# Kernel optimization log

Hardware: AMD Instinct MI355X
Metric: run time of the kernel (lower is better)

Reference implementation:

```python
import jax, jax.numpy as jnp
import numpy as np

BATCH, NEURONS, N_FEAT, IN_DIM, OUT_DIM = 256, 1024, 1024, 256, 128


def setup_inputs() -> dict:
    key = jax.random.key(0)
    kx, kg, kv, kw = jax.random.split(key, 4)
    x = jax.random.normal(kx, (BATCH, N_FEAT, IN_DIM), dtype=jnp.float32)
    G = jax.random.normal(kg, (NEURONS, N_FEAT), dtype=jnp.float32)
    # Original initializes v, w to zeros; use randn so outputs/grads are non-trivial.
    v = jax.random.normal(kv, (NEURONS, IN_DIM, OUT_DIM), dtype=jnp.float32)
    w = jax.random.normal(kw, (NEURONS, IN_DIM, OUT_DIM), dtype=jnp.float32)
    return {"x": x, "G": G, "v": v, "w": w}


def reference(x, G, v, w):
    # Original math: out[i,m] = sum_{j,k,l} G[j,k] * x[i,k,l] * (v - w)[j,l,m]
    # Reordered contraction: first G @ x (sum over feature axis k),
    # avoiding the quadratic (batch, neurons, n, in_dim) intermediate.
    Gx = jnp.einsum('jk,ikl->ijl', G, x)          # (batch, neurons, in_dim)
    return jnp.einsum('ijl,jlm->im', Gx, v - w)    # (batch, out_dim)
```

## Files before the change

### kernel.cpp

```cpp
#include <hip/hip_runtime.h>
#include <hip/hip_bf16.h>


typedef __attribute__((ext_vector_type(8))) short bf16x8;
typedef __attribute__((ext_vector_type(4))) float f32x4;

#define AS1C(p) ((const __attribute__((address_space(1))) void*)(p))
#define AS3(p)  ((__attribute__((address_space(3))) void*)(p))
#define FENCE() asm volatile("" ::: "memory")

__device__ __forceinline__ unsigned short f2bf(float f) {
    unsigned u = __float_as_uint(f);
    unsigned r = u + 0x7fffu + ((u >> 16) & 1u);
    return (unsigned short)(r >> 16);
}

__global__ void prep_G(const float* __restrict__ G, unsigned short* __restrict__ Gt) {
    __shared__ float tile[32][33];
    int k0 = blockIdx.x * 32, j0 = blockIdx.y * 32;
    int tx = threadIdx.x, ty = threadIdx.y;
    #pragma unroll
    for (int r = 0; r < 32; r += 8)
        tile[ty + r][tx] = G[(size_t)(j0 + ty + r) * 1024 + k0 + tx];
    __syncthreads();
    #pragma unroll
    for (int r = 0; r < 32; r += 8)
        Gt[(size_t)(k0 + ty + r) * 1024 + j0 + tx] = f2bf(tile[tx][ty + r]);
}

__global__ void prep_D(const float* __restrict__ v, const float* __restrict__ w,
                       unsigned short* __restrict__ Dt) {
    __shared__ unsigned short tile[32][132];
    int j0 = blockIdx.x * 32;
    int l  = blockIdx.y;
    int t  = threadIdx.x;
    #pragma unroll
    for (int it = 0; it < 16; ++it) {
        int idx = it * 256 + t;
        int j = idx >> 7, m = idx & 127;
        size_t g = (size_t)(j0 + j) * 32768 + (size_t)l * 128 + m;
        tile[j][m] = f2bf(v[g] - w[g]);
    }
    __syncthreads();
    int m = t >> 1, half = t & 1;
    unsigned short vals[16];
    #pragma unroll
    for (int q = 0; q < 16; ++q) vals[q] = tile[half * 16 + q][m];
    size_t dst = ((size_t)m * 256 + l) * 1024 + j0 + half * 16;
    *(uint4*)(Dt + dst)     = *(uint4*)(vals);
    *(uint4*)(Dt + dst + 8) = *(uint4*)(vals + 8);
}

__global__ __launch_bounds__(512, 2) void gemm1(const unsigned short* __restrict__ Gt,
                                                const unsigned short* __restrict__ Dt,
                                                unsigned short* __restrict__ Tt) {
    __shared__ __align__(16) unsigned short sm[65536];
    int tid = threadIdx.x, wv = tid >> 6, lane = tid & 63;
    int n   = blockIdx.x;
    int by  = ((n >> 5) << 3) + (n & 7);
    int bx  = (n >> 3) & 3;
    int k0 = bx * 256, n0 = by * 256;
    int quad = lane >> 4, l15 = lane & 15;
    int wr = (wv >> 2) * 128, wc = (wv & 3) * 64;
    int ldrow = lane >> 2, ldcol = (lane & 3) * 8;
    const unsigned short* gA = Gt + (size_t)k0 * 1024;
    const unsigned short* gB = Dt + (size_t)n0 * 1024;

    f32x4 acc[8][4] = {};

    auto stage = [&](int slot, int jt) {
        int j0 = jt * 32;
        unsigned short* As = sm + slot * 16384;
        unsigned short* Bs = As + 8192;
        #pragma unroll
        for (int i = 0; i < 2; ++i) {
            int r = (wv * 2 + i) * 16;
            __builtin_amdgcn_global_load_lds(
                AS1C(gA + (size_t)(r + ldrow) * 1024 + j0 + ldcol), AS3(As + r * 32), 16, 0, 0);
            __builtin_amdgcn_global_load_lds(
                AS1C(gB + (size_t)(r + ldrow) * 1024 + j0 + ldcol), AS3(Bs + r * 32), 16, 0, 0);
        }
    };

    stage(0, 0);
    stage(1, 1);
    int sR = 0;
    for (int kt = 0; kt < 32; ++kt) {
        if (kt + 1 < 32) asm volatile("s_waitcnt vmcnt(4)" ::: "memory");
        else             asm volatile("s_waitcnt vmcnt(0)" ::: "memory");
        __builtin_amdgcn_s_barrier();
        FENCE();
        if (kt + 2 < 32) {
            int sW = sR + 2; if (sW >= 3) sW -= 3;
            stage(sW, kt + 2);
        }
        const unsigned short* As = sm + sR * 16384;
        const unsigned short* Bs = As + 8192;
        bf16x8 a[8], b[4];
        #pragma unroll
        for (int rt = 0; rt < 8; ++rt)
            a[rt] = *(const bf16x8*)(As + (wr + rt * 16 + l15) * 32 + quad * 8);
        #pragma unroll
        for (int ct = 0; ct < 4; ++ct)
            b[ct] = *(const bf16x8*)(Bs + (wc + ct * 16 + l15) * 32 + quad * 8);
        __builtin_amdgcn_s_setprio(1);
        #pragma unroll
        for (int rt = 0; rt < 8; ++rt)
            #pragma unroll
            for (int ct = 0; ct < 4; ++ct)
                acc[rt][ct] = __builtin_amdgcn_mfma_f32_16x16x32_bf16(a[rt], b[ct], acc[rt][ct], 0, 0, 0);
        __builtin_amdgcn_s_setprio(0);
        sR = sR + 1; if (sR >= 3) sR = 0;
    }

    FENCE();
    __builtin_amdgcn_s_barrier();
    FENCE();
    #pragma unroll
    for (int rt = 0; rt < 8; ++rt)
        #pragma unroll
        for (int ct = 0; ct < 4; ++ct)
            #pragma unroll
            for (int r = 0; r < 4; ++r) {
                int row = wr + rt * 16 + quad * 4 + r;
                int col = wc + ct * 16 + l15;
                int byt = row * 512 + ((col * 2) ^ (((row >> 2) & 3) << 5));
                *(unsigned short*)((char*)sm + byt) = f2bf(acc[rt][ct][r]);
            }
    asm volatile("s_waitcnt lgkmcnt(0)" ::: "memory");
    __builtin_amdgcn_s_barrier();
    FENCE();
    int mm = n0 >> 8;
    size_t base = (size_t)mm * 262144 + (size_t)k0 * 256;
    #pragma unroll
    for (int u = 0; u < 16; ++u) {
        int c = u * 512 + tid;
        int row = c >> 5, col16 = c & 31;
        int byt = row * 512 + ((col16 * 16) ^ (((row >> 2) & 3) << 5));
        *(uint4*)(Tt + base + (size_t)c * 8) = *(const uint4*)((const char*)sm + byt);
    }
}

__global__ __launch_bounds__(256, 4) void gemm2(const float* __restrict__ x,
                                                const unsigned short* __restrict__ Tt,
                                                float* __restrict__ out) {
    __shared__ __align__(16) unsigned short sm[4 * 4096 + 2 * 2048];
    int tid = threadIdx.x, wv = tid >> 6, lane = tid & 63;
    int n   = blockIdx.x;
    int by  = ((n >> 5) << 3) + (n & 7);
    int bx  = (n >> 3) & 3;
    int i0 = bx * 64;
    size_t kl0 = (size_t)by * 1024;
    int ldrow = lane >> 2, ldcol = (lane & 3) * 8;
    int wr = (wv >> 1) * 32, wc = (wv & 1) * 64;
    int quad = lane >> 4, l15 = lane & 15;

    f32x4 acc[2][4] = {};
    float4 xv[2];

    auto stageT = [&](int slot, int t) {
        size_t kk = kl0 + (size_t)t * 32;
        unsigned short* Ts = sm + slot * 4096;
        #pragma unroll
        for (int i = 0; i < 2; ++i) {
            int r = (wv * 2 + i) * 16;
            __builtin_amdgcn_global_load_lds(
                AS1C(Tt + (size_t)(r + ldrow) * 262144 + kk + ldcol), AS3(Ts + r * 32), 16, 0, 0);
        }
    };
    auto loadX = [&](int t) {
        size_t kk = kl0 + (size_t)t * 32;
        #pragma unroll
        for (int i = 0; i < 2; ++i) {
            int f = tid + i * 256;
            int r = f >> 3, c = (f & 7) * 4;
            xv[i] = *(const float4*)(x + (size_t)(i0 + r) * 262144 + kk + c);
        }
    };

    loadX(0);
    stageT(0, 0);
    stageT(1, 1);

    for (int kt = 0; kt < 32; ++kt) {
        if (kt + 1 < 32) asm volatile("s_waitcnt vmcnt(2)" ::: "memory");
        else             asm volatile("s_waitcnt vmcnt(0)" ::: "memory");
        unsigned short* Xw = sm + 16384 + (kt & 1) * 2048;
        #pragma unroll
        for (int i = 0; i < 2; ++i) {
            int f = tid + i * 256;
            int r = f >> 3, c = (f & 7) * 4;
            unsigned short h[4] = {f2bf(xv[i].x), f2bf(xv[i].y), f2bf(xv[i].z), f2bf(xv[i].w)};
            *(uint2*)(Xw + r * 32 + c) = *(uint2*)h;
        }
        asm volatile("s_waitcnt lgkmcnt(0)" ::: "memory");
        __builtin_amdgcn_s_barrier();
        FENCE();
        if (kt + 1 < 32) loadX(kt + 1);
        if (kt + 2 < 32) stageT((kt + 2) & 3, kt + 2);
        const unsigned short* Xs = sm + 16384 + (kt & 1) * 2048;
        const unsigned short* Ts = sm + (kt & 3) * 4096;
        bf16x8 a[2], b[4];
        #pragma unroll
        for (int rt = 0; rt < 2; ++rt)
            a[rt] = *(const bf16x8*)(Xs + (wr + rt * 16 + l15) * 32 + quad * 8);
        #pragma unroll
        for (int ct = 0; ct < 4; ++ct)
            b[ct] = *(const bf16x8*)(Ts + (wc + ct * 16 + l15) * 32 + quad * 8);
        #pragma unroll
        for (int rt = 0; rt < 2; ++rt)
            #pragma unroll
            for (int ct = 0; ct < 4; ++ct)
                acc[rt][ct] = __builtin_amdgcn_mfma_f32_16x16x32_bf16(a[rt], b[ct], acc[rt][ct], 0, 0, 0);
    }
    #pragma unroll
    for (int rt = 0; rt < 2; ++rt)
        #pragma unroll
        for (int ct = 0; ct < 4; ++ct)
            #pragma unroll
            for (int r = 0; r < 4; ++r) {
                int i  = i0 + wr + rt * 16 + quad * 4 + r;
                int mo = wc + ct * 16 + l15;
                atomicAdd(&out[(size_t)i * 128 + mo], acc[rt][ct][r]);
            }
}

extern "C" void kernel_launch(void* const* d_in, const int* in_sizes, int n_in,
                              void* d_out, int out_size, void* d_ws, size_t ws_size,
                              hipStream_t stream) {
    const float* x = (const float*)d_in[0];
    const float* G = (const float*)d_in[1];
    const float* v = (const float*)d_in[2];
    const float* w = (const float*)d_in[3];
    float* out = (float*)d_out;

    char* ws = (char*)d_ws;
    unsigned short* Dt = (unsigned short*)(ws);
    unsigned short* Tt = (unsigned short*)(ws + 67108864);
    unsigned short* Gt = (unsigned short*)(ws + 134217728);

    hipMemsetAsync(d_out, 0, (size_t)256 * 128 * sizeof(float), stream);
    prep_G<<<dim3(32, 32), dim3(32, 8), 0, stream>>>(G, Gt);
    prep_D<<<dim3(32, 256), 256, 0, stream>>>(v, w, Dt);
    gemm1<<<512, 512, 0, stream>>>(Gt, Dt, Tt);
    gemm2<<<1024, 256, 0, stream>>>(x, Tt, out);
}
```

Baseline: 659.2 us.

## Store LDS tiles in MFMA fragment order and vectorize prep_D loads

Changes the global-to-LDS load mapping in both GEMMs so each 16-row block is stored in MFMA operand fragment order. Each lane can then read its bf16x8 fragment at a contiguous offset (lane*8), which is meant to remove LDS bank conflicts from the old row-stride-32 layout. The X conversion store in gemm2 is remapped to match. prep_D now reads v and w as float4 and writes packed bf16 quads to cut its memory instruction count. The global access pattern changes, since each lane group now covers 16 rows times 16 bytes instead of 4 contiguous chunks per row, which may reduce coalescing.

```diff
diff --git a/kernel.cpp b/kernel.cpp
--- a/kernel.cpp
+++ b/kernel.cpp
@@ -35,11 +35,15 @@
     int l  = blockIdx.y;
     int t  = threadIdx.x;
     #pragma unroll
-    for (int it = 0; it < 16; ++it) {
-        int idx = it * 256 + t;
-        int j = idx >> 7, m = idx & 127;
-        size_t g = (size_t)(j0 + j) * 32768 + (size_t)l * 128 + m;
-        tile[j][m] = f2bf(v[g] - w[g]);
+    for (int it = 0; it < 4; ++it) {
+        int id = it * 256 + t;
+        int j = id >> 5, m4 = (id & 31) * 4;
+        size_t g = (size_t)(j0 + j) * 32768 + (size_t)l * 128 + m4;
+        float4 a = *(const float4*)(v + g);
+        float4 b = *(const float4*)(w + g);
+        unsigned short h[4] = {f2bf(a.x - b.x), f2bf(a.y - b.y),
+                               f2bf(a.z - b.z), f2bf(a.w - b.w)};
+        *(uint2*)(&tile[j][m4]) = *(uint2*)h;
     }
     __syncthreads();
     int m = t >> 1, half = t & 1;
@@ -62,7 +66,7 @@
     int k0 = bx * 256, n0 = by * 256;
     int quad = lane >> 4, l15 = lane & 15;
     int wr = (wv >> 2) * 128, wc = (wv & 3) * 64;
-    int ldrow = lane >> 2, ldcol = (lane & 3) * 8;
+    int ldrow = lane & 15, ldcol = (lane >> 4) * 8;
     const unsigned short* gA = Gt + (size_t)k0 * 1024;
     const unsigned short* gB = Dt + (size_t)n0 * 1024;
 
@@ -74,11 +78,12 @@
         unsigned short* Bs = As + 8192;
         #pragma unroll
         for (int i = 0; i < 2; ++i) {
-            int r = (wv * 2 + i) * 16;
+            int rb = wv * 2 + i;
+            int r  = rb * 16;
             __builtin_amdgcn_global_load_lds(
-                AS1C(gA + (size_t)(r + ldrow) * 1024 + j0 + ldcol), AS3(As + r * 32), 16, 0, 0);
+                AS1C(gA + (size_t)(r + ldrow) * 1024 + j0 + ldcol), AS3(As + rb * 512), 16, 0, 0);
             __builtin_amdgcn_global_load_lds(
-                AS1C(gB + (size_t)(r + ldrow) * 1024 + j0 + ldcol), AS3(Bs + r * 32), 16, 0, 0);
+                AS1C(gB + (size_t)(r + ldrow) * 1024 + j0 + ldcol), AS3(Bs + rb * 512), 16, 0, 0);
         }
     };
 
@@ -99,10 +104,10 @@
         bf16x8 a[8], b[4];
         #pragma unroll
         for (int rt = 0; rt < 8; ++rt)
-            a[rt] = *(const bf16x8*)(As + (wr + rt * 16 + l15) * 32 + quad * 8);
-        #pragma unroll
-        for (int ct = 0; ct < 4; ++ct)
-            b[ct] = *(const bf16x8*)(Bs + (wc + ct * 16 + l15) * 32 + quad * 8);
+            a[rt] = *(const bf16x8*)(As + ((wr >> 4) + rt) * 512 + lane * 8);
+        #pragma unroll
+        for (int ct = 0; ct < 4; ++ct)
+            b[ct] = *(const bf16x8*)(Bs + ((wc >> 4) + ct) * 512 + lane * 8);
         __builtin_amdgcn_s_setprio(1);
         #pragma unroll
         for (int rt = 0; rt < 8; ++rt)
@@ -151,7 +156,7 @@
     int bx  = (n >> 3) & 3;
     int i0 = bx * 64;
     size_t kl0 = (size_t)by * 1024;
-    int ldrow = lane >> 2, ldcol = (lane & 3) * 8;
+    int ldrow = lane & 15, ldcol = (lane >> 4) * 8;
     int wr = (wv >> 1) * 32, wc = (wv & 1) * 64;
     int quad = lane >> 4, l15 = lane & 15;
 
@@ -163,9 +168,10 @@
         unsigned short* Ts = sm + slot * 4096;
         #pragma unroll
         for (int i = 0; i < 2; ++i) {
-            int r = (wv * 2 + i) * 16;
+            int rb = wv * 2 + i;
             __builtin_amdgcn_global_load_lds(
-                AS1C(Tt + (size_t)(r + ldrow) * 262144 + kk + ldcol), AS3(Ts + r * 32), 16, 0, 0);
+                AS1C(Tt + (size_t)(rb * 16 + ldrow) * 262144 + kk + ldcol),
+                AS3(Ts + rb * 512), 16, 0, 0);
         }
     };
     auto loadX = [&](int t) {
@@ -191,7 +197,8 @@
             int f = tid + i * 256;
             int r = f >> 3, c = (f & 7) * 4;
             unsigned short h[4] = {f2bf(xv[i].x), f2bf(xv[i].y), f2bf(xv[i].z), f2bf(xv[i].w)};
-            *(uint2*)(Xw + r * 32 + c) = *(uint2*)h;
+            int off = (r >> 4) * 512 + ((c >> 3) * 16 + (r & 15)) * 8 + (c & 7);
+            *(uint2*)(Xw + off) = *(uint2*)h;
         }
         asm volatile("s_waitcnt lgkmcnt(0)" ::: "memory");
         __builtin_amdgcn_s_barrier();
@@ -203,10 +210,10 @@
         bf16x8 a[2], b[4];
         #pragma unroll
         for (int rt = 0; rt < 2; ++rt)
-            a[rt] = *(const bf16x8*)(Xs + (wr + rt * 16 + l15) * 32 + quad * 8);
-        #pragma unroll
-        for (int ct = 0; ct < 4; ++ct)
-            b[ct] = *(const bf16x8*)(Ts + (wc + ct * 16 + l15) * 32 + quad * 8);
+            a[rt] = *(const bf16x8*)(Xs + ((wr >> 4) + rt) * 512 + lane * 8);
+        #pragma unroll
+        for (int ct = 0; ct < 4; ++ct)
+            b[ct] = *(const bf16x8*)(Ts + ((wc >> 4) + ct) * 512 + lane * 8);
         #pragma unroll
         for (int rt = 0; rt < 2; ++rt)
             #pragma unroll
```

Result: no change. 664.8 us (+0.8%).
